# Performance work log

Hardware: AMD Instinct MI355X
Metric: run time of the kernel (lower is better)

The kernel has to match this reference:

```python
import jax, jax.numpy as jnp
import numpy as np

BN_EPS = 1e-5
N_NODES = 100000
N_EDGES = 1600000
D = 128


def setup_inputs() -> dict:
    key = jax.random.key(0)
    ks = jax.random.split(key, 8)
    h = jax.random.normal(ks[0], (N_NODES, D), dtype=jnp.float32)
    snorm_n = jax.random.uniform(ks[1], (N_NODES, 1), dtype=jnp.float32)
    eps = jnp.zeros((1,), dtype=jnp.float32)
    W1 = jax.random.normal(ks[2], (D, D), dtype=jnp.float32) * (1.0 / np.sqrt(D))
    b1 = jnp.zeros((D,), dtype=jnp.float32)
    W2 = jax.random.normal(ks[3], (D, D), dtype=jnp.float32) * (1.0 / np.sqrt(D))
    b2 = jnp.zeros((D,), dtype=jnp.float32)
    bn_gamma = jnp.ones((D,), dtype=jnp.float32)
    bn_beta = jnp.zeros((D,), dtype=jnp.float32)
    src = jax.random.randint(ks[4], (N_EDGES,), 0, N_NODES, dtype=jnp.int32)
    dst = jax.random.randint(ks[5], (N_EDGES,), 0, N_NODES, dtype=jnp.int32)
    return {"h": h, "snorm_n": snorm_n, "eps": eps, "W1": W1, "b1": b1,
            "W2": W2, "b2": b2, "bn_gamma": bn_gamma, "bn_beta": bn_beta,
            "src": src, "dst": dst}


def reference(h, snorm_n, eps, W1, b1, W2, b2, bn_gamma, bn_beta, src, dst):
    h_in = h
    # message passing: copy_u + sum reduce -> scatter-add of h[src] into dst
    neigh = jax.ops.segment_sum(h[src], dst, num_segments=N_NODES)  # [N, D]
    x = (1.0 + eps[0]) * h + neigh
    # apply_func: 2-layer MLP (Linear -> ReLU -> Linear)
    x = jax.nn.relu(x @ W1 + b1) @ W2 + b2
    # graph norm w.r.t. graph sizes
    x = x * snorm_n
    # batch norm (training-mode batch statistics over nodes)
    mean = jnp.mean(x, axis=0)
    var = jnp.var(x, axis=0)
    x = (x - mean) * jax.lax.rsqrt(var + BN_EPS) * bn_gamma + bn_beta
    x = jax.nn.relu(x)
    # residual (in_dim == out_dim)
    x = h_in + x
    # dropout p=0.0 -> identity
    return x
```

## Files before the change

### kernel.cpp

```cpp
#include <hip/hip_runtime.h>

#define D 128
#define NN 100000
#define NE 1600000
#define TILE_R 32
#define SCAN_NBLK 98

__global__ __launch_bounds__(256) void count_kernel(
    const int* __restrict__ dst, int* __restrict__ cnt)
{
    int e = blockIdx.x * 256 + threadIdx.x;
    if (e < NE) atomicAdd(&cnt[dst[e]], 1);
}

__global__ __launch_bounds__(256) void scan_local_kernel(
    const int* __restrict__ cnt, int* __restrict__ pre, int* __restrict__ blkSum)
{
    __shared__ int lds[256];
    const int t = threadIdx.x;
    const int base = blockIdx.x * 1024 + t * 4;
    int4 v = {0, 0, 0, 0};
    if (base + 3 < NN) v = *(const int4*)&cnt[base];
    else {
        if (base + 0 < NN) v.x = cnt[base + 0];
        if (base + 1 < NN) v.y = cnt[base + 1];
        if (base + 2 < NN) v.z = cnt[base + 2];
        if (base + 3 < NN) v.w = cnt[base + 3];
    }
    const int s = v.x + v.y + v.z + v.w;
    lds[t] = s;
    __syncthreads();
    for (int off = 1; off < 256; off <<= 1) {
        int val = 0;
        if (t >= off) val = lds[t - off];
        __syncthreads();
        if (t >= off) lds[t] += val;
        __syncthreads();
    }
    const int excl = lds[t] - s;
    if (t == 255) blkSum[blockIdx.x] = lds[255];
    int4 o;
    o.x = excl;
    o.y = excl + v.x;
    o.z = excl + v.x + v.y;
    o.w = excl + v.x + v.y + v.z;
    if (base + 3 < NN) *(int4*)&pre[base] = o;
    else {
        if (base + 0 < NN) pre[base + 0] = o.x;
        if (base + 1 < NN) pre[base + 1] = o.y;
        if (base + 2 < NN) pre[base + 2] = o.z;
        if (base + 3 < NN) pre[base + 3] = o.w;
    }
}

__global__ __launch_bounds__(128) void scan_blk_kernel(
    const int* __restrict__ blkSum, int* __restrict__ blkOfs)
{
    __shared__ int lds[128];
    const int t = threadIdx.x;
    int s = (t < SCAN_NBLK) ? blkSum[t] : 0;
    lds[t] = s;
    __syncthreads();
    for (int off = 1; off < 128; off <<= 1) {
        int val = 0;
        if (t >= off) val = lds[t - off];
        __syncthreads();
        if (t >= off) lds[t] += val;
        __syncthreads();
    }
    blkOfs[t] = lds[t] - s;
}

__global__ __launch_bounds__(256) void scan_finish_kernel(
    const int* __restrict__ pre, const int* __restrict__ blkOfs,
    int* __restrict__ row_start, int* __restrict__ cursor)
{
    int n = blockIdx.x * 256 + threadIdx.x;
    if (n > NN) return;
    int v = (n == NN) ? NE : pre[n] + blkOfs[n >> 10];
    row_start[n] = v;
    if (n < NN) cursor[n] = v;
}

__global__ __launch_bounds__(256) void fill_kernel(
    const int* __restrict__ src, const int* __restrict__ dst,
    int* __restrict__ cursor, int* __restrict__ eidx)
{
    int e = blockIdx.x * 256 + threadIdx.x;
    if (e >= NE) return;
    int pos = atomicAdd(&cursor[dst[e]], 1);
    eidx[pos] = src[e];
}

__global__ __launch_bounds__(256) void gather_kernel(
    const float* __restrict__ h, const int* __restrict__ row_start,
    const int* __restrict__ eidx, const float* __restrict__ epsp,
    float* __restrict__ x)
{
    int gid  = blockIdx.x * 256 + threadIdx.x;
    int node = gid >> 5;
    int lane = gid & 31;
    if (node >= NN) return;
    const int s0 = row_start[node];
    const int s1 = row_start[node + 1];
    const float sc = 1.0f + epsp[0];
    float4 hv = ((const float4*)(h + (size_t)node * D))[lane];
    float ax = sc * hv.x, ay = sc * hv.y, az = sc * hv.z, aw = sc * hv.w;
    for (int e = s0; e < s1; ++e) {
        int s = eidx[e];
        float4 v = ((const float4*)(h + (size_t)s * D))[lane];
        ax += v.x; ay += v.y; az += v.z; aw += v.w;
    }
    float4 o = {ax, ay, az, aw};
    ((float4*)(x + (size_t)node * D))[lane] = o;
}

template <int MODE>
__global__ __launch_bounds__(256) void mlp_gemm_kernel(
    const float* __restrict__ xin, const float* __restrict__ W,
    const float* __restrict__ bias, const float* __restrict__ snorm,
    float* __restrict__ out)
{
    __shared__ float w_lds[D][D];
    __shared__ float xs[TILE_R][D];
    const int tid = threadIdx.x;

    {
        const float4* Wv = (const float4*)W;
        float4* wv = (float4*)w_lds;
#pragma unroll
        for (int i = 0; i < (D * D / 4) / 256; ++i)
            wv[tid + i * 256] = Wv[tid + i * 256];
    }
    const int row0 = blockIdx.x * TILE_R;
    {
        const float4* Av = (const float4*)(xin + (size_t)row0 * D);
        float4* xv = (float4*)xs;
#pragma unroll
        for (int i = 0; i < (TILE_R * D / 4) / 256; ++i)
            xv[tid + i * 256] = Av[tid + i * 256];
    }
    __syncthreads();

    const int cg = tid & 15;
    const int rg = tid >> 4;
    const int c0 = cg * 8;
    const int r0 = rg * 2;

    float acc[2][8];
#pragma unroll
    for (int i = 0; i < 2; ++i)
#pragma unroll
        for (int j = 0; j < 8; ++j) acc[i][j] = 0.0f;

#pragma unroll 4
    for (int k0 = 0; k0 < D; k0 += 4) {
        float4 xa = *(const float4*)&xs[r0][k0];
        float4 xb = *(const float4*)&xs[r0 + 1][k0];
        float xav[4] = {xa.x, xa.y, xa.z, xa.w};
        float xbv[4] = {xb.x, xb.y, xb.z, xb.w};
#pragma unroll
        for (int kk = 0; kk < 4; ++kk) {
            float4 w0 = *(const float4*)&w_lds[k0 + kk][c0];
            float4 w1 = *(const float4*)&w_lds[k0 + kk][c0 + 4];
            float wv[8] = {w0.x, w0.y, w0.z, w0.w, w1.x, w1.y, w1.z, w1.w};
            float va = xav[kk], vb = xbv[kk];
#pragma unroll
            for (int j = 0; j < 8; ++j) {
                acc[0][j] = fmaf(va, wv[j], acc[0][j]);
                acc[1][j] = fmaf(vb, wv[j], acc[1][j]);
            }
        }
    }

    float bv[8];
    *(float4*)&bv[0] = *(const float4*)&bias[c0];
    *(float4*)&bv[4] = *(const float4*)&bias[c0 + 4];
#pragma unroll
    for (int i = 0; i < 2; ++i) {
        const int row = row0 + r0 + i;
        float o[8];
        if (MODE == 1) {
#pragma unroll
            for (int j = 0; j < 8; ++j) o[j] = fmaxf(acc[i][j] + bv[j], 0.0f);
        } else {
            const float sn = snorm[row];
#pragma unroll
            for (int j = 0; j < 8; ++j) o[j] = (acc[i][j] + bv[j]) * sn;
        }
        float4* op = (float4*)(out + (size_t)row * D + c0);
        op[0] = *(float4*)&o[0];
        op[1] = *(float4*)&o[4];
    }
}

__global__ __launch_bounds__(256) void bn_stats_kernel(
    const float* __restrict__ y, double* __restrict__ stats)
{
    __shared__ float ssum[D], ssq[D];
    const int tid = threadIdx.x;
    if (tid < D) { ssum[tid] = 0.0f; ssq[tid] = 0.0f; }
    __syncthreads();
    const int rw = tid >> 5;
    const int cf = tid & 31;
    const int r0 = blockIdx.x * 256;
    const int rend = (r0 + 256 < NN) ? r0 + 256 : NN;
    float s0 = 0, s1 = 0, s2 = 0, s3 = 0, q0 = 0, q1 = 0, q2 = 0, q3 = 0;
    for (int r = r0 + rw; r < rend; r += 8) {
        float4 v = *(const float4*)&y[(size_t)r * D + (size_t)cf * 4];
        s0 += v.x; s1 += v.y; s2 += v.z; s3 += v.w;
        q0 += v.x * v.x; q1 += v.y * v.y; q2 += v.z * v.z; q3 += v.w * v.w;
    }
    atomicAdd(&ssum[cf * 4 + 0], s0);
    atomicAdd(&ssum[cf * 4 + 1], s1);
    atomicAdd(&ssum[cf * 4 + 2], s2);
    atomicAdd(&ssum[cf * 4 + 3], s3);
    atomicAdd(&ssq[cf * 4 + 0], q0);
    atomicAdd(&ssq[cf * 4 + 1], q1);
    atomicAdd(&ssq[cf * 4 + 2], q2);
    atomicAdd(&ssq[cf * 4 + 3], q3);
    __syncthreads();
    if (tid < D) {
        atomicAdd(&stats[tid], (double)ssum[tid]);
        atomicAdd(&stats[D + tid], (double)ssq[tid]);
    }
}

__global__ void bn_prep_kernel(const double* __restrict__ stats,
                               const float* __restrict__ gamma,
                               const float* __restrict__ beta,
                               float* __restrict__ sc_sh)
{
    int c = threadIdx.x;
    double mean = stats[c] * (1.0 / NN);
    double var  = stats[D + c] * (1.0 / NN) - mean * mean;
    float rs = rsqrtf((float)var + 1e-5f);
    float sc = gamma[c] * rs;
    sc_sh[c]     = sc;
    sc_sh[D + c] = beta[c] - (float)mean * sc;
}

__global__ __launch_bounds__(256) void finalize_kernel(
    const float* __restrict__ y, const float* __restrict__ h,
    const float* __restrict__ sc_sh, float* __restrict__ out)
{
    int i  = blockIdx.x * 256 + threadIdx.x;
    int cf = i & 31;
    float4 yv = ((const float4*)y)[i];
    float4 hv = ((const float4*)h)[i];
    float4 sc = ((const float4*)sc_sh)[cf];
    float4 sh = ((const float4*)(sc_sh + D))[cf];
    float4 o;
    o.x = hv.x + fmaxf(fmaf(yv.x, sc.x, sh.x), 0.0f);
    o.y = hv.y + fmaxf(fmaf(yv.y, sc.y, sh.y), 0.0f);
    o.z = hv.z + fmaxf(fmaf(yv.z, sc.z, sh.z), 0.0f);
    o.w = hv.w + fmaxf(fmaf(yv.w, sc.w, sh.w), 0.0f);
    ((float4*)out)[i] = o;
}

extern "C" void kernel_launch(void* const* d_in, const int* in_sizes, int n_in,
                              void* d_out, int out_size, void* d_ws, size_t ws_size,
                              hipStream_t stream)
{
    const float* h     = (const float*)d_in[0];
    const float* snorm = (const float*)d_in[1];
    const float* eps   = (const float*)d_in[2];
    const float* W1    = (const float*)d_in[3];
    const float* b1    = (const float*)d_in[4];
    const float* W2    = (const float*)d_in[5];
    const float* b2    = (const float*)d_in[6];
    const float* gamma = (const float*)d_in[7];
    const float* beta  = (const float*)d_in[8];
    const int*   src   = (const int*)d_in[9];
    const int*   dst   = (const int*)d_in[10];
    float* out = (float*)d_out;

    char* ws = (char*)d_ws;
    const size_t BUF_BYTES = (size_t)NN * D * sizeof(float);
    float*  buf       = (float*)ws;
    double* stats     = (double*)(ws + BUF_BYTES);
    float*  sc_sh     = (float*)(ws + BUF_BYTES + 2048);
    char*   p         = ws + BUF_BYTES + 4096;
    int*    cnt       = (int*)p;            p += (size_t)NN * 4;
    int*    pre       = (int*)p;            p += (size_t)NN * 4;
    int*    row_start = (int*)p;            p += (size_t)(NN + 4) * 4;
    int*    cursor    = (int*)p;            p += (size_t)NN * 4;
    int*    blkSum    = (int*)p;            p += 512;
    int*    blkOfs    = (int*)p;            p += 512;
    int*    eidx      = (int*)p;

    hipMemsetAsync(cnt, 0, (size_t)NN * 4, stream);
    hipMemsetAsync(stats, 0, 2048, stream);

    count_kernel<<<(NE + 255) / 256, 256, 0, stream>>>(dst, cnt);
    scan_local_kernel<<<SCAN_NBLK, 256, 0, stream>>>(cnt, pre, blkSum);
    scan_blk_kernel<<<1, 128, 0, stream>>>(blkSum, blkOfs);
    scan_finish_kernel<<<(NN + 256) / 256, 256, 0, stream>>>(pre, blkOfs, row_start, cursor);
    fill_kernel<<<(NE + 255) / 256, 256, 0, stream>>>(src, dst, cursor, eidx);

    gather_kernel<<<NN * 32 / 256, 256, 0, stream>>>(h, row_start, eidx, eps, buf);

    mlp_gemm_kernel<1><<<NN / TILE_R, 256, 0, stream>>>(buf, W1, b1, nullptr, buf);
    mlp_gemm_kernel<2><<<NN / TILE_R, 256, 0, stream>>>(buf, W2, b2, snorm, buf);

    bn_stats_kernel<<<(NN + 255) / 256, 256, 0, stream>>>(buf, stats);
    bn_prep_kernel<<<1, D, 0, stream>>>(stats, gamma, beta, sc_sh);
    finalize_kernel<<<NN * D / 4 / 256, 256, 0, stream>>>(buf, h, sc_sh, out);
}
```

Baseline: 600.5 us.

## Use persistent register-tiled GEMM with prefetch and fused BN statistics

Result: faster. 566.2 us (-5.7%).

```diff
diff --git a/kernel.cpp b/kernel.cpp
--- a/kernel.cpp
+++ b/kernel.cpp
@@ -3,14 +3,21 @@
 #define D 128
 #define NN 100000
 #define NE 1600000
-#define TILE_R 32
 #define SCAN_NBLK 98
+#define GT_ROWS 128
+#define GEMM_NT ((NN + GT_ROWS - 1) / GT_ROWS)
+#define GEMM_GRID 256
 
 __global__ __launch_bounds__(256) void count_kernel(
     const int* __restrict__ dst, int* __restrict__ cnt)
 {
-    int e = blockIdx.x * 256 + threadIdx.x;
-    if (e < NE) atomicAdd(&cnt[dst[e]], 1);
+    int g4 = blockIdx.x * 256 + threadIdx.x;
+    if (g4 >= NE / 4) return;
+    int4 d = ((const int4*)dst)[g4];
+    atomicAdd(&cnt[d.x], 1);
+    atomicAdd(&cnt[d.y], 1);
+    atomicAdd(&cnt[d.z], 1);
+    atomicAdd(&cnt[d.w], 1);
 }
 
 __global__ __launch_bounds__(256) void scan_local_kernel(
@@ -106,123 +113,187 @@
     const float sc = 1.0f + epsp[0];
     float4 hv = ((const float4*)(h + (size_t)node * D))[lane];
     float ax = sc * hv.x, ay = sc * hv.y, az = sc * hv.z, aw = sc * hv.w;
-    for (int e = s0; e < s1; ++e) {
-        int s = eidx[e];
-        float4 v = ((const float4*)(h + (size_t)s * D))[lane];
-        ax += v.x; ay += v.y; az += v.z; aw += v.w;
-    }
-    float4 o = {ax, ay, az, aw};
+    float bx = 0.f, by = 0.f, bz = 0.f, bw = 0.f;
+    int e = s0;
+    for (; e + 1 < s1; e += 2) {
+        int sa = eidx[e];
+        int sb = eidx[e + 1];
+        float4 va = ((const float4*)(h + (size_t)sa * D))[lane];
+        float4 vb = ((const float4*)(h + (size_t)sb * D))[lane];
+        ax += va.x; ay += va.y; az += va.z; aw += va.w;
+        bx += vb.x; by += vb.y; bz += vb.z; bw += vb.w;
+    }
+    if (e < s1) {
+        int sa = eidx[e];
+        float4 va = ((const float4*)(h + (size_t)sa * D))[lane];
+        ax += va.x; ay += va.y; az += va.z; aw += va.w;
+    }
+    float4 o = {ax + bx, ay + by, az + bz, aw + bw};
     ((float4*)(x + (size_t)node * D))[lane] = o;
 }
 
 template <int MODE>
-__global__ __launch_bounds__(256) void mlp_gemm_kernel(
+__global__ __launch_bounds__(256, 1) void gemm_kernel(
     const float* __restrict__ xin, const float* __restrict__ W,
     const float* __restrict__ bias, const float* __restrict__ snorm,
-    float* __restrict__ out)
-{
-    __shared__ float w_lds[D][D];
-    __shared__ float xs[TILE_R][D];
+    float* __restrict__ out, double* __restrict__ stats)
+{
+    __shared__ float wl[D * D];
+    __shared__ float xb[D * GT_ROWS];
     const int tid = threadIdx.x;
 
     {
         const float4* Wv = (const float4*)W;
-        float4* wv = (float4*)w_lds;
-#pragma unroll
-        for (int i = 0; i < (D * D / 4) / 256; ++i)
-            wv[tid + i * 256] = Wv[tid + i * 256];
-    }
-    const int row0 = blockIdx.x * TILE_R;
-    {
-        const float4* Av = (const float4*)(xin + (size_t)row0 * D);
-        float4* xv = (float4*)xs;
-#pragma unroll
-        for (int i = 0; i < (TILE_R * D / 4) / 256; ++i)
-            xv[tid + i * 256] = Av[tid + i * 256];
-    }
-    __syncthreads();
+        float4* wv = (float4*)wl;
+#pragma unroll
+        for (int i = 0; i < 16; ++i) wv[tid + i * 256] = Wv[tid + i * 256];
+    }
 
     const int cg = tid & 15;
     const int rg = tid >> 4;
-    const int c0 = cg * 8;
-    const int r0 = rg * 2;
-
-    float acc[2][8];
-#pragma unroll
-    for (int i = 0; i < 2; ++i)
-#pragma unroll
-        for (int j = 0; j < 8; ++j) acc[i][j] = 0.0f;
-
+    const int ca = cg * 4;
+    const int cb = 64 + cg * 4;
+
+    float4 bva = ((const float4*)bias)[cg];
+    float4 bvb = ((const float4*)bias)[16 + cg];
+
+    float ssum[8], ssq[8];
+#pragma unroll
+    for (int j = 0; j < 8; ++j) { ssum[j] = 0.f; ssq[j] = 0.f; }
+
+    float4 rstg[8];
+    auto LOADH = [&](int t, int hk) {
+        const int row0 = t * GT_ROWS;
+#pragma unroll
+        for (int i = 0; i < 8; ++i) {
+            int idx = tid + i * 256;
+            int row = idx >> 4;
+            int kc  = (idx & 15) + hk * 16;
+            int grow = row0 + row;
+            rstg[i] = (grow < NN)
+                ? ((const float4*)(xin + (size_t)grow * D))[kc]
+                : make_float4(0.f, 0.f, 0.f, 0.f);
+        }
+    };
+    auto WRITEH = [&](int hk) {
+#pragma unroll
+        for (int i = 0; i < 8; ++i) {
+            int idx = tid + i * 256;
+            int row = idx >> 4;
+            int kc  = (idx & 15) + hk * 16;
+            int c4  = (row >> 2) ^ (kc & 7);
+            float v[4] = {rstg[i].x, rstg[i].y, rstg[i].z, rstg[i].w};
+#pragma unroll
+            for (int j = 0; j < 4; ++j)
+                xb[(kc * 4 + j) * GT_ROWS + c4 * 4 + (row & 3)] = v[j];
+        }
+    };
+
+    for (int t = blockIdx.x; t < GEMM_NT; t += GEMM_GRID) {
+        float acc[8][8];
+#pragma unroll
+        for (int i = 0; i < 8; ++i)
+#pragma unroll
+            for (int j = 0; j < 8; ++j) acc[i][j] = 0.f;
+
+        if (t == (int)blockIdx.x) LOADH(t, 0);
+        __syncthreads();
+        WRITEH(0);
+        LOADH(t, 1);
+        __syncthreads();
+
+#pragma unroll 1
+        for (int half = 0; half < 2; ++half) {
+            const int k0 = half * 64;
 #pragma unroll 4
-    for (int k0 = 0; k0 < D; k0 += 4) {
-        float4 xa = *(const float4*)&xs[r0][k0];
-        float4 xb = *(const float4*)&xs[r0 + 1][k0];
-        float xav[4] = {xa.x, xa.y, xa.z, xa.w};
-        float xbv[4] = {xb.x, xb.y, xb.z, xb.w};
-#pragma unroll
-        for (int kk = 0; kk < 4; ++kk) {
-            float4 w0 = *(const float4*)&w_lds[k0 + kk][c0];
-            float4 w1 = *(const float4*)&w_lds[k0 + kk][c0 + 4];
-            float wv[8] = {w0.x, w0.y, w0.z, w0.w, w1.x, w1.y, w1.z, w1.w};
-            float va = xav[kk], vb = xbv[kk];
-#pragma unroll
-            for (int j = 0; j < 8; ++j) {
-                acc[0][j] = fmaf(va, wv[j], acc[0][j]);
-                acc[1][j] = fmaf(vb, wv[j], acc[1][j]);
+            for (int kk = 0; kk < 64; ++kk) {
+                const int k  = k0 + kk;
+                const int sk = (k >> 2) & 7;
+                float4 xa = *(const float4*)&xb[k * GT_ROWS + (((2 * rg) ^ sk) << 2)];
+                float4 xc = *(const float4*)&xb[k * GT_ROWS + (((2 * rg + 1) ^ sk) << 2)];
+                float4 wa = *(const float4*)&wl[k * D + ca];
+                float4 wb = *(const float4*)&wl[k * D + cb];
+                float xr[8] = {xa.x, xa.y, xa.z, xa.w, xc.x, xc.y, xc.z, xc.w};
+                float wr[8] = {wa.x, wa.y, wa.z, wa.w, wb.x, wb.y, wb.z, wb.w};
+#pragma unroll
+                for (int i = 0; i < 8; ++i)
+#pragma unroll
+                    for (int j = 0; j < 8; ++j)
+                        acc[i][j] = fmaf(xr[i], wr[j], acc[i][j]);
             }
-        }
-    }
-
-    float bv[8];
-    *(float4*)&bv[0] = *(const float4*)&bias[c0];
-    *(float4*)&bv[4] = *(const float4*)&bias[c0 + 4];
-#pragma unroll
-    for (int i = 0; i < 2; ++i) {
-        const int row = row0 + r0 + i;
-        float o[8];
-        if (MODE == 1) {
-#pragma unroll
-            for (int j = 0; j < 8; ++j) o[j] = fmaxf(acc[i][j] + bv[j], 0.0f);
-        } else {
-            const float sn = snorm[row];
-#pragma unroll
-            for (int j = 0; j < 8; ++j) o[j] = (acc[i][j] + bv[j]) * sn;
-        }
-        float4* op = (float4*)(out + (size_t)row * D + c0);
-        op[0] = *(float4*)&o[0];
-        op[1] = *(float4*)&o[4];
-    }
-}
-
-__global__ __launch_bounds__(256) void bn_stats_kernel(
-    const float* __restrict__ y, double* __restrict__ stats)
-{
-    __shared__ float ssum[D], ssq[D];
-    const int tid = threadIdx.x;
-    if (tid < D) { ssum[tid] = 0.0f; ssq[tid] = 0.0f; }
-    __syncthreads();
-    const int rw = tid >> 5;
-    const int cf = tid & 31;
-    const int r0 = blockIdx.x * 256;
-    const int rend = (r0 + 256 < NN) ? r0 + 256 : NN;
-    float s0 = 0, s1 = 0, s2 = 0, s3 = 0, q0 = 0, q1 = 0, q2 = 0, q3 = 0;
-    for (int r = r0 + rw; r < rend; r += 8) {
-        float4 v = *(const float4*)&y[(size_t)r * D + (size_t)cf * 4];
-        s0 += v.x; s1 += v.y; s2 += v.z; s3 += v.w;
-        q0 += v.x * v.x; q1 += v.y * v.y; q2 += v.z * v.z; q3 += v.w * v.w;
-    }
-    atomicAdd(&ssum[cf * 4 + 0], s0);
-    atomicAdd(&ssum[cf * 4 + 1], s1);
-    atomicAdd(&ssum[cf * 4 + 2], s2);
-    atomicAdd(&ssum[cf * 4 + 3], s3);
-    atomicAdd(&ssq[cf * 4 + 0], q0);
-    atomicAdd(&ssq[cf * 4 + 1], q1);
-    atomicAdd(&ssq[cf * 4 + 2], q2);
-    atomicAdd(&ssq[cf * 4 + 3], q3);
-    __syncthreads();
-    if (tid < D) {
-        atomicAdd(&stats[tid], (double)ssum[tid]);
-        atomicAdd(&stats[D + tid], (double)ssq[tid]);
+            if (half == 0) {
+                WRITEH(1);
+                int tn = t + GEMM_GRID;
+                if (tn < GEMM_NT) LOADH(tn, 0);
+                __syncthreads();
+            }
+        }
+
+#pragma unroll
+        for (int i = 0; i < 8; ++i) {
+            int row = t * GT_ROWS + rg * 8 + i;
+            if (row < NN) {
+                float oa[4], ob[4];
+                if (MODE == 1) {
+                    oa[0] = fmaxf(acc[i][0] + bva.x, 0.f);
+                    oa[1] = fmaxf(acc[i][1] + bva.y, 0.f);
+                    oa[2] = fmaxf(acc[i][2] + bva.z, 0.f);
+                    oa[3] = fmaxf(acc[i][3] + bva.w, 0.f);
+                    ob[0] = fmaxf(acc[i][4] + bvb.x, 0.f);
+                    ob[1] = fmaxf(acc[i][5] + bvb.y, 0.f);
+                    ob[2] = fmaxf(acc[i][6] + bvb.z, 0.f);
+                    ob[3] = fmaxf(acc[i][7] + bvb.w, 0.f);
+                } else {
+                    const float sn = snorm[row];
+                    oa[0] = (acc[i][0] + bva.x) * sn;
+                    oa[1] = (acc[i][1] + bva.y) * sn;
+                    oa[2] = (acc[i][2] + bva.z) * sn;
+                    oa[3] = (acc[i][3] + bva.w) * sn;
+                    ob[0] = (acc[i][4] + bvb.x) * sn;
+                    ob[1] = (acc[i][5] + bvb.y) * sn;
+                    ob[2] = (acc[i][6] + bvb.z) * sn;
+                    ob[3] = (acc[i][7] + bvb.w) * sn;
+#pragma unroll
+                    for (int j = 0; j < 4; ++j) {
+                        ssum[j]     += oa[j];  ssq[j]     += oa[j] * oa[j];
+                        ssum[4 + j] += ob[j];  ssq[4 + j] += ob[j] * ob[j];
+                    }
+                }
+                float* op = out + (size_t)row * D;
+                *(float4*)&op[ca] = *(float4*)&oa[0];
+                *(float4*)&op[cb] = *(float4*)&ob[0];
+            }
+        }
+    }
+
+    if (MODE == 2) {
+        float* red = xb;
+        __syncthreads();
+#pragma unroll
+        for (int j = 0; j < 4; ++j) {
+            red[rg * D + ca + j] = ssum[j];
+            red[rg * D + cb + j] = ssum[4 + j];
+        }
+        __syncthreads();
+        if (tid < D) {
+            float s = 0.f;
+#pragma unroll
+            for (int r = 0; r < 16; ++r) s += red[r * D + tid];
+            atomicAdd(&stats[tid], (double)s);
+        }
+        __syncthreads();
+#pragma unroll
+        for (int j = 0; j < 4; ++j) {
+            red[rg * D + ca + j] = ssq[j];
+            red[rg * D + cb + j] = ssq[4 + j];
+        }
+        __syncthreads();
+        if (tid < D) {
+            float s = 0.f;
+#pragma unroll
+            for (int r = 0; r < 16; ++r) s += red[r * D + tid];
+            atomicAdd(&stats[D + tid], (double)s);
+        }
     }
 }
 
@@ -292,18 +363,17 @@
     hipMemsetAsync(cnt, 0, (size_t)NN * 4, stream);
     hipMemsetAsync(stats, 0, 2048, stream);
 
-    count_kernel<<<(NE + 255) / 256, 256, 0, stream>>>(dst, cnt);
+    count_kernel<<<(NE / 4 + 255) / 256, 256, 0, stream>>>(dst, cnt);
     scan_local_kernel<<<SCAN_NBLK, 256, 0, stream>>>(cnt, pre, blkSum);
     scan_blk_kernel<<<1, 128, 0, stream>>>(blkSum, blkOfs);
-    scan_finish_kernel<<<(NN + 256) / 256, 256, 0, stream>>>(pre, blkOfs, row_start, cursor);
+    scan_finish_kernel<<<(NN + 256) / 256 + 1, 256, 0, stream>>>(pre, blkOfs, row_start, cursor);
     fill_kernel<<<(NE + 255) / 256, 256, 0, stream>>>(src, dst, cursor, eidx);
 
     gather_kernel<<<NN * 32 / 256, 256, 0, stream>>>(h, row_start, eidx, eps, buf);
 
-    mlp_gemm_kernel<1><<<NN / TILE_R, 256, 0, stream>>>(buf, W1, b1, nullptr, buf);
-    mlp_gemm_kernel<2><<<NN / TILE_R, 256, 0, stream>>>(buf, W2, b2, snorm, buf);
-
-    bn_stats_kernel<<<(NN + 255) / 256, 256, 0, stream>>>(buf, stats);
+    gemm_kernel<1><<<GEMM_GRID, 256, 0, stream>>>(buf, W1, b1, nullptr, buf, nullptr);
+    gemm_kernel<2><<<GEMM_GRID, 256, 0, stream>>>(buf, W2, b2, snorm, buf, stats);
+
     bn_prep_kernel<<<1, D, 0, stream>>>(stats, gamma, beta, sc_sh);
     finalize_kernel<<<NN * D / 4 / 256, 256, 0, stream>>>(buf, h, sc_sh, out);
 }
```
